# Kernel tuning notes

Measured on AMD Instinct MI355X. Metric: run time of the kernel, lower is better.

The kernel has to match this reference:

```python
import jax, jax.numpy as jnp
import numpy as np

NH, NKV, HD, ROPE_DIMS, ROPE_BASE = 16, 4, 128, 64, 10000.0


def _rms_norm(x):
    eps = jnp.asarray(jnp.finfo(x.dtype).eps, x.dtype)
    return x * jax.lax.rsqrt(jnp.mean(x * x, axis=-1, keepdims=True) + eps)


def _apply_rope_partial(x, cos, sin):
    # x: [B, H, T, hd]; cos/sin: [T, rope_dims//2]
    h = ROPE_DIMS // 2
    xa, xb, xp = x[..., :h], x[..., h:ROPE_DIMS], x[..., ROPE_DIMS:]
    c, s = cos[None, None], sin[None, None]
    rot = jnp.concatenate([xa * c - xb * s, xa * s + xb * c], axis=-1)
    return jnp.concatenate([rot, xp], axis=-1)


def setup_inputs() -> dict:
    key = jax.random.key(0)
    ks = jax.random.split(key, 7)
    B, T, D = 2, 2048, 2048
    kv_dim = NKV * HD
    sc = lambda n: 1.0 / np.sqrt(n)
    return {
        "x": jax.random.normal(ks[0], (B, T, D), jnp.float32),
        "ve_embed": jax.random.normal(ks[1], (B, T, kv_dim), jnp.float32),
        "Wq": jax.random.normal(ks[2], (D, D), jnp.float32) * sc(D),
        "Wk": jax.random.normal(ks[3], (kv_dim, D), jnp.float32) * sc(D),
        "Wv": jax.random.normal(ks[4], (kv_dim, D), jnp.float32) * sc(D),
        "Wproj": jax.random.normal(ks[5], (D, D), jnp.float32) * sc(D),
        "q_gain": jnp.full((NH,), 12.0, jnp.float32)
        + 0.01 * jax.random.normal(ks[6], (NH,), jnp.float32),
    }


def reference(x, ve_embed, Wq, Wk, Wv, Wproj, q_gain):
    B, T, D = x.shape
    g = NH // NKV  # GQA group size

    # QKV projections -> [B, H, T, hd]
    q = (x @ Wq.T).reshape(B, T, NH, HD).transpose(0, 2, 1, 3)
    k = (x @ Wk.T).reshape(B, T, NKV, HD).transpose(0, 2, 1, 3)
    v = (x @ Wv.T).reshape(B, T, NKV, HD).transpose(0, 2, 1, 3)

    q, k = _rms_norm(q), _rms_norm(k)

    # partial RoPE (frequencies built over full hd, first rope_dims//2 used)
    inv_freq = 1.0 / ROPE_BASE ** (jnp.arange(0, HD, 2, dtype=jnp.float32) / HD)
    f = jnp.arange(T, dtype=jnp.float32)[:, None] * inv_freq[None, :]  # [T, hd//2]
    cos, sin = jnp.cos(f)[:, : ROPE_DIMS // 2], jnp.sin(f)[:, : ROPE_DIMS // 2]
    q = _apply_rope_partial(q, cos, sin)
    k = _apply_rope_partial(k, cos, sin)

    q = q * q_gain[None, :, None, None]
    v = v + ve_embed.reshape(B, T, NKV, HD).transpose(0, 2, 1, 3)

    # GQA causal attention: q grouped as [B, nkv, g, T, hd]
    qg = q.reshape(B, NKV, g, T, HD)
    scale = 1.0 / np.sqrt(HD)
    scores = jnp.einsum("bkgtd,bksd->bkgts", qg, k) * scale
    causal = jnp.tril(jnp.ones((T, T), bool))
    scores = jnp.where(causal[None, None, None], scores, -jnp.inf)
    p = jax.nn.softmax(scores, axis=-1)
    y = jnp.einsum("bkgts,bksd->bkgtd", p, v)  # [B, nkv, g, T, hd]

    y = y.reshape(B, NH, T, HD).transpose(0, 2, 1, 3).reshape(B, T, D)
    return y @ Wproj.T
```

## Files before the change

kernel.cpp:

```cpp
#include <hip/hip_runtime.h>
#include <hip/hip_bf16.h>
#include <cstdint>
#include <cstddef>


typedef _Float16 f16_t;
typedef f16_t f16x4 __attribute__((ext_vector_type(4)));
typedef f16_t f16x8 __attribute__((ext_vector_type(8)));
typedef float f32x4 __attribute__((ext_vector_type(4)));

#define MFMA16F(a, b, c) __builtin_amdgcn_mfma_f32_16x16x32_f16((a), (b), (c), 0, 0, 0)
#define SBAR()   __builtin_amdgcn_s_barrier()
#define SCHED0() __builtin_amdgcn_sched_barrier(0)
#define LGKM0()  asm volatile("s_waitcnt lgkmcnt(0)" ::: "memory")

__device__ __forceinline__ void gload16(const f16_t* g, f16_t* l) {
  auto lds_ptr = reinterpret_cast<__attribute__((address_space(3))) unsigned int*>(
      reinterpret_cast<uintptr_t>(l));
  auto g_ptr = reinterpret_cast<const __attribute__((address_space(1))) unsigned int*>(
      reinterpret_cast<uintptr_t>(g));
  __builtin_amdgcn_global_load_lds(g_ptr, lds_ptr, 16, 0, 0);
}

__global__ void k_cast_f16(const float* __restrict__ in, f16_t* __restrict__ o, long n) {
  long i = ((long)blockIdx.x * blockDim.x + threadIdx.x) * 4;
  const long step = (long)gridDim.x * blockDim.x * 4;
  for (; i < n; i += step) {
    const float4 v = *reinterpret_cast<const float4*>(in + i);
    f16_t r[4] = {(f16_t)v.x, (f16_t)v.y, (f16_t)v.z, (f16_t)v.w};
    *reinterpret_cast<uint64_t*>(o + i) = *reinterpret_cast<const uint64_t*>(r);
  }
}

__global__ void k_cast_wqkv(const float* __restrict__ Wq, const float* __restrict__ Wk,
                            const float* __restrict__ Wv, f16_t* __restrict__ wf) {
  long i = ((long)blockIdx.x * blockDim.x + threadIdx.x) * 4;
  const long step = (long)gridDim.x * blockDim.x * 4;
  for (; i < (long)3072 * 2048; i += step) {
    const long row = i >> 11, col = i & 2047;
    const float* src = (row < 2048) ? (Wq + (size_t)row * 2048)
                     : (row < 2560) ? (Wk + (size_t)(row - 2048) * 2048)
                                    : (Wv + (size_t)(row - 2560) * 2048);
    const float4 v = *reinterpret_cast<const float4*>(src + col);
    f16_t r[4] = {(f16_t)v.x, (f16_t)v.y, (f16_t)v.z, (f16_t)v.w};
    *reinterpret_cast<uint64_t*>(wf + row * 2048 + col) = *reinterpret_cast<const uint64_t*>(r);
  }
}

__global__ void k_rope_tab(float* __restrict__ ctab, float* __restrict__ stab) {
  const int idx = blockIdx.x * blockDim.x + threadIdx.x;
  if (idx >= 2048 * 32) return;
  const int t = idx >> 5, i = idx & 31;
  const float freq = exp2f(-(float)i * 0.2076205059304601f);
  const float f = (float)t * freq;
  ctab[idx] = cosf(f);
  stab[idx] = sinf(f);
}

__global__ __launch_bounds__(256) void k_vtrans(
    const f16_t* __restrict__ vn, f16_t* __restrict__ vt)
{
  __shared__ __align__(16) f16_t lsT[64 * 136];
  const int t0 = blockIdx.x * 64;
  const int bk = blockIdx.y;
  const f16_t* src = vn + ((size_t)bk * 2048 + t0) * 128;
  f16_t* dst = vt + (size_t)bk * 128 * 2048;
  const int tid = threadIdx.x;
#pragma unroll
  for (int it = 0; it < 4; ++it) {
    const int cch = tid + it * 256;
    const int r = cch >> 4, c = cch & 15;
    *reinterpret_cast<f16x8*>(&lsT[r * 136 + c * 8]) =
        *reinterpret_cast<const f16x8*>(src + (size_t)r * 128 + c * 8);
  }
  __syncthreads();
#pragma unroll
  for (int it = 0; it < 4; ++it) {
    const int u = tid + it * 256;
    const int d = u >> 3, c8 = u & 7;
    f16_t vals[8];
#pragma unroll
    for (int j = 0; j < 8; ++j) vals[j] = lsT[(c8 * 8 + j) * 136 + d];
    *reinterpret_cast<f16x8*>(dst + (size_t)d * 2048 + t0 + c8 * 8) =
        *reinterpret_cast<const f16x8*>(vals);
  }
}

template <int NBU, typename OutT>
__global__ __launch_bounds__(1024, 1) void k_gemmQ(
    const f16_t* __restrict__ A, const f16_t* __restrict__ Bm,
    OutT* __restrict__ C, int M, int N, int K, int lda, int ldb)
{
  __shared__ __align__(16) f16_t lds[2][(4 + NBU) * 4096];
  const int tid = threadIdx.x;
  const int l = tid & 63, w = tid >> 6;
  const int lrow = l & 15, lk = l >> 4;
  const int wm = w >> 2, wn = w & 3;

  const int nwg = gridDim.x * gridDim.y;
  int lin = blockIdx.y * gridDim.x + blockIdx.x;
  lin = (lin & 7) * (nwg >> 3) + (lin >> 3);
  const int m0 = (lin / gridDim.x) * 256, n0 = (lin % gridDim.x) * (64 * NBU);

  const bool stager = (tid < 512);
  const int srow = tid >> 3;
  const int scol = ((tid & 7) ^ (srow & 7)) << 3;
  const f16_t* gP[4 + NBU];
#pragma unroll
  for (int u = 0; u < 4; ++u) gP[u] = A + (size_t)(m0 + u * 64 + srow) * lda + scol;
#pragma unroll
  for (int u = 0; u < NBU; ++u) gP[4 + u] = Bm + (size_t)(n0 + u * 64 + srow) * ldb + scol;

  auto stageAll = [&](int buf, int k0) {
#pragma unroll
    for (int u = 0; u < 4 + NBU; ++u)
      gload16(gP[u] + k0, &lds[buf][u * 4096 + tid * 8]);
  };
  auto rdA = [&](int buf, int mf, int ks) -> f16x8 {
    const int row = wm * 64 + mf * 16 + lrow;
    const int slot = ((ks << 2) | lk) ^ (row & 7);
    return *reinterpret_cast<const f16x8*>(&lds[buf][row * 64 + slot * 8]);
  };
  auto rdB = [&](int buf, int nf, int ks) -> f16x8 {
    const int row = wn * (16 * NBU) + nf * 16 + lrow;
    const int slot = ((ks << 2) | lk) ^ (row & 7);
    return *reinterpret_cast<const f16x8*>(&lds[buf][16384 + row * 64 + slot * 8]);
  };

  f32x4 acc[4][NBU] = {};
  const int nkt = K >> 6;

  if (stager) {
    stageAll(0, 0);
    stageAll(1, nkt > 1 ? 64 : 0);
  }
  if constexpr (NBU == 3) { asm volatile("s_waitcnt vmcnt(7)" ::: "memory"); }
  else                    { asm volatile("s_waitcnt vmcnt(6)" ::: "memory"); }
  SCHED0();
  SBAR(); SCHED0();

  f16x8 aA[4][2], bB[NBU][2];
  for (int kt = 0; kt < nkt; ++kt) {
    const int b = kt & 1;
    const int kn2 = (kt + 2 < nkt ? kt + 2 : nkt - 1) << 6;

#pragma unroll
    for (int mf = 0; mf < 4; ++mf) { aA[mf][0] = rdA(b, mf, 0); aA[mf][1] = rdA(b, mf, 1); }
#pragma unroll
    for (int nf = 0; nf < NBU; ++nf) { bB[nf][0] = rdB(b, nf, 0); bB[nf][1] = rdB(b, nf, 1); }
    __builtin_amdgcn_s_setprio(1);
#pragma unroll
    for (int mf = 0; mf < 2; ++mf)
#pragma unroll
      for (int nf = 0; nf < NBU; ++nf)
#pragma unroll
        for (int ks = 0; ks < 2; ++ks)
          acc[mf][nf] = MFMA16F(aA[mf][ks], bB[nf][ks], acc[mf][nf]);
    __builtin_amdgcn_s_setprio(0);
    LGKM0(); SCHED0();
    SBAR(); SCHED0();

    if (stager) stageAll(b, kn2);
    if constexpr (NBU == 3) { asm volatile("s_waitcnt vmcnt(7)" ::: "memory"); }
    else                    { asm volatile("s_waitcnt vmcnt(6)" ::: "memory"); }
    SCHED0();
    __builtin_amdgcn_s_setprio(1);
#pragma unroll
    for (int mf = 2; mf < 4; ++mf)
#pragma unroll
      for (int nf = 0; nf < NBU; ++nf)
#pragma unroll
        for (int ks = 0; ks < 2; ++ks)
          acc[mf][nf] = MFMA16F(aA[mf][ks], bB[nf][ks], acc[mf][nf]);
    __builtin_amdgcn_s_setprio(0);
    SBAR(); SCHED0();
  }

#pragma unroll
  for (int mf = 0; mf < 4; ++mf) {
    const int row = m0 + wm * 64 + mf * 16 + lk * 4;
#pragma unroll
    for (int nf = 0; nf < NBU; ++nf) {
      const int col = n0 + wn * (16 * NBU) + nf * 16 + lrow;
#pragma unroll
      for (int rg = 0; rg < 4; ++rg)
        C[(size_t)(row + rg) * N + col] = (OutT)acc[mf][nf][rg];
    }
  }
  (void)M;
}

__global__ __launch_bounds__(256) void k_qkv_epi(
    const f16_t* __restrict__ qkv, const float* __restrict__ ve,
    const float* __restrict__ qgain,
    const float* __restrict__ ctab, const float* __restrict__ stab,
    f16_t* __restrict__ qn, f16_t* __restrict__ kn, f16_t* __restrict__ vn)
{
  const int blk = blockIdx.x;
  const int b = blk >> 11, t = blk & 2047;
  const int w = threadIdx.x >> 6, l = threadIdx.x & 63;
  const int i32 = l & 31;
  const float c = ctab[t * 32 + i32], s = stab[t * 32 + i32];
  const float EPS = 1.1920929e-07f;
  constexpr float SCALE_L2E = 0.088388347648318447f * 1.4426950408889634f;

#pragma unroll
  for (int it = 0; it < 4; ++it) {
    const int h = w + it * 4;
    const f16_t* row = qkv + (size_t)blk * 3072 + h * 128;
    float x0 = (float)row[l], x1 = (float)row[l + 64];
    float ss = x0 * x0 + x1 * x1;
#pragma unroll
    for (int off = 32; off; off >>= 1) ss += __shfl_xor(ss, off);
    const float rn = rsqrtf(ss * (1.0f / 128.0f) + EPS);
    x0 *= rn; x1 *= rn;
    const float p = __shfl_xor(x0, 32);
    float xr = (l < 32) ? (x0 * c - p * s) : (p * s + x0 * c);
    const float g = qgain[h] * SCALE_L2E;
    xr *= g; x1 *= g;
    f16_t* orow = qn + (((size_t)(b * 16 + h)) * 2048 + t) * 128;
    orow[l] = (f16_t)xr;
    orow[l + 64] = (f16_t)x1;
  }
  {
    const f16_t* row = qkv + (size_t)blk * 3072 + 2048 + w * 128;
    float x0 = (float)row[l], x1 = (float)row[l + 64];
    float ss = x0 * x0 + x1 * x1;
#pragma unroll
    for (int off = 32; off; off >>= 1) ss += __shfl_xor(ss, off);
    const float rn = rsqrtf(ss * (1.0f / 128.0f) + EPS);
    x0 *= rn; x1 *= rn;
    const float p = __shfl_xor(x0, 32);
    const float xr = (l < 32) ? (x0 * c - p * s) : (p * s + x0 * c);
    f16_t* orow = kn + (((size_t)(b * 4 + w)) * 2048 + t) * 128;
    orow[l] = (f16_t)xr;
    orow[l + 64] = (f16_t)x1;
  }
  {
    const f16_t* row = qkv + (size_t)blk * 3072 + 2560 + w * 128;
    const float* verow = ve + (size_t)blk * 512 + w * 128;
    f16_t* orow = vn + (((size_t)(b * 4 + w)) * 2048 + t) * 128;
    orow[l] = (f16_t)((float)row[l] + verow[l]);
    orow[l + 64] = (f16_t)((float)row[l + 64] + verow[l + 64]);
  }
}

__global__ __launch_bounds__(256, 3) void k_attn(
    const f16_t* __restrict__ qn, const f16_t* __restrict__ kn,
    const f16_t* __restrict__ vt, f16_t* __restrict__ y)
{
  __shared__ __align__(16) f16_t lsK[64 * 128];
  __shared__ __align__(16) f16_t lsV[128 * 64];
  __shared__ __align__(16) f16_t lsPb[4][16 * 64];
  const int qt = 31 - (int)blockIdx.y;
  const int bh = blockIdx.x;
  const int b = bh >> 4, h = bh & 15, kvh = h >> 2;
  const int tid = threadIdx.x, w = tid >> 6, l = tid & 63;
  const int lrow = l & 15, lk = l >> 4;
  const int qbase = qt * 64 + w * 16;
  constexpr float NEG = -1e30f;
  f16_t* lsP = lsPb[w];

  const f16_t* qp = qn + ((size_t)(b * 16 + h) * 2048) * 128;
  f16x8 aQ[4];
#pragma unroll
  for (int kf = 0; kf < 4; ++kf)
    aQ[kf] = *reinterpret_cast<const f16x8*>(
        qp + (size_t)(qbase + lrow) * 128 + kf * 32 + lk * 8);

  const f16_t* kp = kn + ((size_t)(b * 4 + kvh) * 2048) * 128;
  const f16_t* vtp = vt + (size_t)(b * 4 + kvh) * 128 * 2048;

  f32x4 o[8] = {};
  float mst = NEG;
  float lst = 0.f;

  f16x8 kreg[4], vreg[4];
  auto loadKV = [&](int t0) {
#pragma unroll
    for (int it = 0; it < 4; ++it) {
      const int cch = tid + it * 256;
      kreg[it] = *reinterpret_cast<const f16x8*>(
          kp + (size_t)(t0 + (cch >> 4)) * 128 + (cch & 15) * 8);
      vreg[it] = *reinterpret_cast<const f16x8*>(
          vtp + (size_t)(cch >> 3) * 2048 + t0 + (cch & 7) * 8);
    }
  };
  loadKV(0);

  const int ntiles = qt + 1;
  for (int tt = 0; tt < ntiles; ++tt) {
    __syncthreads();
#pragma unroll
    for (int it = 0; it < 4; ++it) {
      const int cch = tid + it * 256;
      const int r = cch >> 4, dg = cch & 15;
      *reinterpret_cast<f16x8*>(&lsK[r * 128 + ((dg ^ (r & 7)) << 3)]) = kreg[it];
      const int d = cch >> 3, c8 = cch & 7;
      *reinterpret_cast<f16x8*>(&lsV[d * 64 + ((c8 ^ ((d >> 3) & 7)) << 3)]) = vreg[it];
    }
    if (tt + 1 < ntiles) loadKV((tt + 1) * 64);
    __syncthreads();

    f32x4 sacc[4] = {};
#pragma unroll
    for (int cf = 0; cf < 4; ++cf) {
      const int krow = cf * 16 + lrow;
#pragma unroll
      for (int kf = 0; kf < 4; ++kf) {
        const f16x8 aK = *reinterpret_cast<const f16x8*>(
            &lsK[krow * 128 + ((((kf << 2) | lk) ^ (krow & 7)) << 3)]);
        sacc[cf] = MFMA16F(aK, aQ[kf], sacc[cf]);
      }
    }

    if (tt == qt) {
      const int qin = w * 16 + lrow;
#pragma unroll
      for (int cf = 0; cf < 4; ++cf)
#pragma unroll
        for (int rg = 0; rg < 4; ++rg)
          if (cf * 16 + lk * 4 + rg > qin) sacc[cf][rg] = NEG;
    }

    float mx = NEG;
#pragma unroll
    for (int cf = 0; cf < 4; ++cf)
      mx = fmaxf(mx, fmaxf(fmaxf(sacc[cf][0], sacc[cf][1]),
                           fmaxf(sacc[cf][2], sacc[cf][3])));
    if (__any(mx > mst + 8.f)) {
      float rmx = mx;
      rmx = fmaxf(rmx, __shfl_xor(rmx, 16));
      rmx = fmaxf(rmx, __shfl_xor(rmx, 32));
      const float mnew = fmaxf(mst, rmx);
      const float alpha = exp2f(mst - mnew);
      mst = mnew;
      lst *= alpha;
#pragma unroll
      for (int rg = 0; rg < 4; ++rg) {
        const float arow = __shfl(alpha, lk * 4 + rg);
#pragma unroll
        for (int df = 0; df < 8; ++df) o[df][rg] *= arow;
      }
    }
#pragma unroll
    for (int cf = 0; cf < 4; ++cf) {
#pragma unroll
      for (int rg = 0; rg < 4; ++rg) {
        const float p = exp2f(sacc[cf][rg] - mst);
        sacc[cf][rg] = p;
        lst += p;
      }
    }

#pragma unroll
    for (int cf = 0; cf < 4; ++cf) {
      f16x4 pk;
#pragma unroll
      for (int rg = 0; rg < 4; ++rg) pk[rg] = (f16_t)sacc[cf][rg];
      const int slot8 = cf * 2 + (lk >> 1);
      *reinterpret_cast<f16x4*>(
          &lsP[lrow * 64 + ((slot8 ^ (lrow & 7)) << 3) + (lk & 1) * 4]) = pk;
    }
#pragma unroll
    for (int k2 = 0; k2 < 2; ++k2) {
      const f16x8 aP = *reinterpret_cast<const f16x8*>(
          &lsP[lrow * 64 + ((((k2 << 2) | lk) ^ (lrow & 7)) << 3)]);
#pragma unroll
      for (int df = 0; df < 8; ++df) {
        const int row = df * 16 + lrow;
        const f16x8 bV = *reinterpret_cast<const f16x8*>(
            &lsV[row * 64 + ((((k2 << 2) | lk) ^ ((row >> 3) & 7)) << 3)]);
        o[df] = MFMA16F(aP, bV, o[df]);
      }
    }
  }

  lst += __shfl_xor(lst, 16);
  lst += __shfl_xor(lst, 32);

#pragma unroll
  for (int rg = 0; rg < 4; ++rg) {
    const float lrow_sum = __shfl(lst, lk * 4 + rg);
    const float inv = 1.0f / lrow_sum;
    const int qi = qbase + lk * 4 + rg;
    const size_t rowoff = ((size_t)(b * 2048 + qi)) * 2048 + h * 128;
#pragma unroll
    for (int df = 0; df < 8; ++df)
      y[rowoff + df * 16 + lrow] = (f16_t)(o[df][rg] * inv);
  }
}

extern "C" void kernel_launch(void* const* d_in, const int* in_sizes, int n_in,
                              void* d_out, int out_size, void* d_ws, size_t ws_size,
                              hipStream_t stream) {
  const float* x  = (const float*)d_in[0];
  const float* ve = (const float*)d_in[1];
  const float* Wq = (const float*)d_in[2];
  const float* Wk = (const float*)d_in[3];
  const float* Wv = (const float*)d_in[4];
  const float* Wp = (const float*)d_in[5];
  const float* qg = (const float*)d_in[6];
  float* out = (float*)d_out;

  char* ws = (char*)d_ws;
  size_t off = 0;
  auto alloc = [&](size_t bytes) -> char* {
    char* p = ws + off;
    off += (bytes + 255) & ~(size_t)255;
    return p;
  };

  f16_t* xf    = (f16_t*)alloc((size_t)4096 * 2048 * 2);
  f16_t* wqkvf = (f16_t*)alloc((size_t)3072 * 2048 * 2);
  f16_t* wpf   = (f16_t*)alloc((size_t)2048 * 2048 * 2);
  f16_t* qkvf  = (f16_t*)alloc((size_t)4096 * 3072 * 2);
  f16_t* kn    = (f16_t*)alloc((size_t)2 * 4 * 2048 * 128 * 2);
  f16_t* vn    = (f16_t*)alloc((size_t)2 * 4 * 2048 * 128 * 2);
  f16_t* vt    = (f16_t*)alloc((size_t)2 * 4 * 128 * 2048 * 2);
  float* ctab  = (float*)alloc((size_t)2048 * 32 * 4);
  float* stab  = (float*)alloc((size_t)2048 * 32 * 4);
  f16_t* qn    = xf;
  f16_t* yb    = qkvf;
  (void)ws_size; (void)in_sizes; (void)n_in; (void)out_size;

  k_cast_f16<<<1024, 256, 0, stream>>>(x, xf, (long)4096 * 2048);
  k_cast_wqkv<<<1536, 256, 0, stream>>>(Wq, Wk, Wv, wqkvf);
  k_cast_f16<<<1024, 256, 0, stream>>>(Wp, wpf, (long)2048 * 2048);
  k_rope_tab<<<256, 256, 0, stream>>>(ctab, stab);

  k_gemmQ<3, f16_t><<<dim3(16, 16), 1024, 0, stream>>>(
      xf, wqkvf, qkvf, 4096, 3072, 2048, 2048, 2048);

  k_qkv_epi<<<4096, 256, 0, stream>>>(qkvf, ve, qg, ctab, stab, qn, kn, vn);

  k_vtrans<<<dim3(32, 8), 256, 0, stream>>>(vn, vt);

  k_attn<<<dim3(32, 32), 256, 0, stream>>>(qn, kn, vt, yb);

  k_gemmQ<2, float><<<dim3(16, 16), 1024, 0, stream>>>(
      yb, wpf, out, 4096, 2048, 2048, 2048, 2048);
}
```

Measured before the change: 207.0 us.

## Double query tile per attention block to reuse K/V tiles across two query fragments

Each attention block now covers 128 query rows instead of 64, and each wave holds two 16-row query fragments. Every K/V tile loaded into LDS therefore feeds twice as many MFMAs, halving K/V global traffic and LDS fill work per query. Causal masking is reworked for the two diagonal tiles, and waves 0-1 skip the last tile. The V LDS swizzle pattern also changes. The cost is more registers (launch bounds relaxed from 3 to 2 blocks per CU), half as many blocks, and coarser load balance across the causal triangle.

```diff
diff --git a/kernel.cpp b/kernel.cpp
--- a/kernel.cpp
+++ b/kernel.cpp
@@ -245,35 +245,35 @@
   }
 }
 
-__global__ __launch_bounds__(256, 3) void k_attn(
+__global__ __launch_bounds__(256, 2) void k_attn(
     const f16_t* __restrict__ qn, const f16_t* __restrict__ kn,
     const f16_t* __restrict__ vt, f16_t* __restrict__ y)
 {
   __shared__ __align__(16) f16_t lsK[64 * 128];
   __shared__ __align__(16) f16_t lsV[128 * 64];
-  __shared__ __align__(16) f16_t lsPb[4][16 * 64];
-  const int qt = 31 - (int)blockIdx.y;
+  __shared__ __align__(16) f16_t lsPb[4][2][16 * 64];
+  const int qt = 15 - (int)blockIdx.y;
   const int bh = blockIdx.x;
   const int b = bh >> 4, h = bh & 15, kvh = h >> 2;
   const int tid = threadIdx.x, w = tid >> 6, l = tid & 63;
   const int lrow = l & 15, lk = l >> 4;
-  const int qbase = qt * 64 + w * 16;
+  const int qbase = qt * 128 + w * 32;
   constexpr float NEG = -1e30f;
-  f16_t* lsP = lsPb[w];
 
   const f16_t* qp = qn + ((size_t)(b * 16 + h) * 2048) * 128;
-  f16x8 aQ[4];
-#pragma unroll
-  for (int kf = 0; kf < 4; ++kf)
-    aQ[kf] = *reinterpret_cast<const f16x8*>(
-        qp + (size_t)(qbase + lrow) * 128 + kf * 32 + lk * 8);
+  f16x8 bQ[2][4];
+#pragma unroll
+  for (int qf = 0; qf < 2; ++qf)
+#pragma unroll
+    for (int kf = 0; kf < 4; ++kf)
+      bQ[qf][kf] = *reinterpret_cast<const f16x8*>(
+          qp + (size_t)(qbase + qf * 16 + lrow) * 128 + kf * 32 + lk * 8);
 
   const f16_t* kp = kn + ((size_t)(b * 4 + kvh) * 2048) * 128;
   const f16_t* vtp = vt + (size_t)(b * 4 + kvh) * 128 * 2048;
 
-  f32x4 o[8] = {};
-  float mst = NEG;
-  float lst = 0.f;
+  f32x4 o0[8] = {}, o1[8] = {};
+  float mst0 = NEG, mst1 = NEG, lst0 = 0.f, lst1 = 0.f;
 
   f16x8 kreg[4], vreg[4];
   auto loadKV = [&](int t0) {
@@ -288,7 +288,7 @@
   };
   loadKV(0);
 
-  const int ntiles = qt + 1;
+  const int ntiles = 2 * qt + 2;
   for (int tt = 0; tt < ntiles; ++tt) {
     __syncthreads();
 #pragma unroll
@@ -297,12 +297,14 @@
       const int r = cch >> 4, dg = cch & 15;
       *reinterpret_cast<f16x8*>(&lsK[r * 128 + ((dg ^ (r & 7)) << 3)]) = kreg[it];
       const int d = cch >> 3, c8 = cch & 7;
-      *reinterpret_cast<f16x8*>(&lsV[d * 64 + ((c8 ^ ((d >> 3) & 7)) << 3)]) = vreg[it];
+      *reinterpret_cast<f16x8*>(&lsV[d * 64 + ((c8 ^ (d & 7)) << 3)]) = vreg[it];
     }
     if (tt + 1 < ntiles) loadKV((tt + 1) * 64);
     __syncthreads();
 
-    f32x4 sacc[4] = {};
+    if (tt == 2 * qt + 1 && w < 2) continue;
+
+    f32x4 sacc0[4] = {}, sacc1[4] = {};
 #pragma unroll
     for (int cf = 0; cf < 4; ++cf) {
       const int krow = cf * 16 + lrow;
@@ -310,84 +312,107 @@
       for (int kf = 0; kf < 4; ++kf) {
         const f16x8 aK = *reinterpret_cast<const f16x8*>(
             &lsK[krow * 128 + ((((kf << 2) | lk) ^ (krow & 7)) << 3)]);
-        sacc[cf] = MFMA16F(aK, aQ[kf], sacc[cf]);
+        sacc0[cf] = MFMA16F(aK, bQ[0][kf], sacc0[cf]);
+        sacc1[cf] = MFMA16F(aK, bQ[1][kf], sacc1[cf]);
       }
     }
 
-    if (tt == qt) {
-      const int qin = w * 16 + lrow;
+    if (tt >= 2 * qt) {
+      const int kvoff = (tt - 2 * qt) * 64;
 #pragma unroll
       for (int cf = 0; cf < 4; ++cf)
 #pragma unroll
-        for (int rg = 0; rg < 4; ++rg)
-          if (cf * 16 + lk * 4 + rg > qin) sacc[cf][rg] = NEG;
-    }
-
-    float mx = NEG;
-#pragma unroll
-    for (int cf = 0; cf < 4; ++cf)
-      mx = fmaxf(mx, fmaxf(fmaxf(sacc[cf][0], sacc[cf][1]),
-                           fmaxf(sacc[cf][2], sacc[cf][3])));
-    if (__any(mx > mst + 8.f)) {
-      float rmx = mx;
-      rmx = fmaxf(rmx, __shfl_xor(rmx, 16));
-      rmx = fmaxf(rmx, __shfl_xor(rmx, 32));
-      const float mnew = fmaxf(mst, rmx);
-      const float alpha = exp2f(mst - mnew);
-      mst = mnew;
-      lst *= alpha;
-#pragma unroll
-      for (int rg = 0; rg < 4; ++rg) {
-        const float arow = __shfl(alpha, lk * 4 + rg);
-#pragma unroll
-        for (int df = 0; df < 8; ++df) o[df][rg] *= arow;
+        for (int rg = 0; rg < 4; ++rg) {
+          const int kvl = kvoff + cf * 16 + lk * 4 + rg;
+          if (kvl > w * 32 + lrow) sacc0[cf][rg] = NEG;
+          if (kvl > w * 32 + 16 + lrow) sacc1[cf][rg] = NEG;
+        }
+    }
+
+#pragma unroll
+    for (int qf = 0; qf < 2; ++qf) {
+      f32x4* sacc = qf ? sacc1 : sacc0;
+      float& mst = qf ? mst1 : mst0;
+      float& lst = qf ? lst1 : lst0;
+      f32x4* o = qf ? o1 : o0;
+
+      float mx = NEG;
+#pragma unroll
+      for (int cf = 0; cf < 4; ++cf)
+        mx = fmaxf(mx, fmaxf(fmaxf(sacc[cf][0], sacc[cf][1]),
+                             fmaxf(sacc[cf][2], sacc[cf][3])));
+      if (__any(mx > mst + 8.f)) {
+        float rmx = mx;
+        rmx = fmaxf(rmx, __shfl_xor(rmx, 16));
+        rmx = fmaxf(rmx, __shfl_xor(rmx, 32));
+        const float mnew = fmaxf(mst, rmx);
+        const float alpha = exp2f(mst - mnew);
+        mst = mnew;
+        lst *= alpha;
+#pragma unroll
+        for (int rg = 0; rg < 4; ++rg) {
+          const float arow = __shfl(alpha, lk * 4 + rg);
+#pragma unroll
+          for (int df = 0; df < 8; ++df) o[df][rg] *= arow;
+        }
       }
-    }
-#pragma unroll
-    for (int cf = 0; cf < 4; ++cf) {
-#pragma unroll
-      for (int rg = 0; rg < 4; ++rg) {
-        const float p = exp2f(sacc[cf][rg] - mst);
-        sacc[cf][rg] = p;
-        lst += p;
+#pragma unroll
+      for (int cf = 0; cf < 4; ++cf) {
+#pragma unroll
+        for (int rg = 0; rg < 4; ++rg) {
+          const float p = exp2f(sacc[cf][rg] - mst);
+          sacc[cf][rg] = p;
+          lst += p;
+        }
       }
-    }
-
-#pragma unroll
-    for (int cf = 0; cf < 4; ++cf) {
-      f16x4 pk;
-#pragma unroll
-      for (int rg = 0; rg < 4; ++rg) pk[rg] = (f16_t)sacc[cf][rg];
-      const int slot8 = cf * 2 + (lk >> 1);
-      *reinterpret_cast<f16x4*>(
-          &lsP[lrow * 64 + ((slot8 ^ (lrow & 7)) << 3) + (lk & 1) * 4]) = pk;
-    }
+      f16_t* lsP = lsPb[w][qf];
+#pragma unroll
+      for (int cf = 0; cf < 4; ++cf) {
+        f16x4 pk;
+#pragma unroll
+        for (int rg = 0; rg < 4; ++rg) pk[rg] = (f16_t)sacc[cf][rg];
+        const int slot8 = cf * 2 + (lk >> 1);
+        *reinterpret_cast<f16x4*>(
+            &lsPb[w][qf][lrow * 64 + ((slot8 ^ (lrow & 7)) << 3) + (lk & 1) * 4]) = pk;
+      }
+      (void)lsP;
+    }
+
 #pragma unroll
     for (int k2 = 0; k2 < 2; ++k2) {
-      const f16x8 aP = *reinterpret_cast<const f16x8*>(
-          &lsP[lrow * 64 + ((((k2 << 2) | lk) ^ (lrow & 7)) << 3)]);
+      const int pofs = lrow * 64 + ((((k2 << 2) | lk) ^ (lrow & 7)) << 3);
+      const f16x8 aP0 = *reinterpret_cast<const f16x8*>(&lsPb[w][0][pofs]);
+      const f16x8 aP1 = *reinterpret_cast<const f16x8*>(&lsPb[w][1][pofs]);
 #pragma unroll
       for (int df = 0; df < 8; ++df) {
         const int row = df * 16 + lrow;
         const f16x8 bV = *reinterpret_cast<const f16x8*>(
-            &lsV[row * 64 + ((((k2 << 2) | lk) ^ ((row >> 3) & 7)) << 3)]);
-        o[df] = MFMA16F(aP, bV, o[df]);
+            &lsV[row * 64 + ((((k2 << 2) | lk) ^ (row & 7)) << 3)]);
+        o0[df] = MFMA16F(aP0, bV, o0[df]);
+        o1[df] = MFMA16F(aP1, bV, o1[df]);
       }
     }
   }
 
-  lst += __shfl_xor(lst, 16);
-  lst += __shfl_xor(lst, 32);
-
-#pragma unroll
-  for (int rg = 0; rg < 4; ++rg) {
-    const float lrow_sum = __shfl(lst, lk * 4 + rg);
-    const float inv = 1.0f / lrow_sum;
-    const int qi = qbase + lk * 4 + rg;
-    const size_t rowoff = ((size_t)(b * 2048 + qi)) * 2048 + h * 128;
-#pragma unroll
-    for (int df = 0; df < 8; ++df)
-      y[rowoff + df * 16 + lrow] = (f16_t)(o[df][rg] * inv);
+  lst0 += __shfl_xor(lst0, 16);
+  lst0 += __shfl_xor(lst0, 32);
+  lst1 += __shfl_xor(lst1, 16);
+  lst1 += __shfl_xor(lst1, 32);
+
+#pragma unroll
+  for (int qf = 0; qf < 2; ++qf) {
+    const f32x4* o = qf ? o1 : o0;
+    const float lstq = qf ? lst1 : lst0;
+#pragma unroll
+    for (int rg = 0; rg < 4; ++rg) {
+      const float lrow_sum = __shfl(lstq, lk * 4 + rg);
+      const float inv = 1.0f / lrow_sum;
+      const int qi = qbase + qf * 16 + lk * 4 + rg;
+      const size_t rowoff = ((size_t)(b * 2048 + qi)) * 2048 + h * 128;
+#pragma unroll
+      for (int df = 0; df < 8; ++df)
+        y[rowoff + df * 16 + lrow] = (f16_t)(o[df][rg] * inv);
+    }
   }
 }
 
@@ -436,7 +461,7 @@
 
   k_vtrans<<<dim3(32, 8), 256, 0, stream>>>(vn, vt);
 
-  k_attn<<<dim3(32, 32), 256, 0, stream>>>(qn, kn, vt, yb);
+  k_attn<<<dim3(32, 16), 256, 0, stream>>>(qn, kn, vt, yb);
 
   k_gemmQ<2, float><<<dim3(16, 16), 1024, 0, stream>>>(
       yb, wpf, out, 4096, 2048, 2048, 2048, 2048);
```

Result: faster. 198.5 us (-4.1%).
